# Performance work log

Hardware: AMD Instinct MI355X
Metric: run time of the kernel (lower is better)

Reference implementation:

```python
import jax, jax.numpy as jnp
import numpy as np

B, NPG, A, E = 128, 512, 8, 504   # graphs, nodes/graph, agents, edges/graph
F_IN, HID, H = 3, 64, 8
C = HID
F = H * C                          # 512 = concat head output
OUT = 2
NEG_SLOPE = 0.2


def _seg_softmax(alpha, dst, n):
    # edge-softmax normalized over destination-node neighborhoods
    m = jax.ops.segment_max(alpha, dst, num_segments=n)
    e = jnp.exp(alpha - m[dst])
    s = jax.ops.segment_sum(e, dst, num_segments=n)
    return e / jnp.clip(s[dst], 1e-16)


def _gat(x, src, dst, ea, W, b, a_s, a_d, We, a_e, n, self_loops):
    # PyG GATConv: heads=H, concat=True, edge_dim=1, fill_value='mean'
    xs = (x @ W).reshape(n, H, C)                      # [N,H,C]
    als = jnp.einsum('nhc,hc->nh', xs, a_s)            # alpha_src per node
    ald = jnp.einsum('nhc,hc->nh', xs, a_d)            # alpha_dst per node
    if self_loops:
        # fill_value='mean': self-loop attr = mean of incoming edge attrs
        ssum = jax.ops.segment_sum(ea, dst, num_segments=n)
        cnt = jax.ops.segment_sum(jnp.ones((dst.shape[0], 1), ea.dtype), dst, num_segments=n)
        loop_attr = ssum / jnp.maximum(cnt, 1.0)
        ea = jnp.concatenate([ea, loop_attr], axis=0)
        loop = jnp.arange(n, dtype=src.dtype)
        src = jnp.concatenate([src, loop])
        dst = jnp.concatenate([dst, loop])
    ee = (ea @ We).reshape(-1, H, C)                   # lin_edge
    ale = jnp.einsum('ehc,hc->eh', ee, a_e)            # alpha_edge per edge
    alpha = jax.nn.leaky_relu(als[src] + ald[dst] + ale, NEG_SLOPE)  # [E,H]
    alpha = _seg_softmax(alpha, dst, n)
    out = jax.ops.segment_sum(alpha[:, :, None] * xs[src], dst, num_segments=n)
    return out.reshape(n, H * C) + b


def _forward(x, edge_index, edge_attr, p1, p2, p3, fc1_w, fc1_b, fc2_w, fc2_b):
    Bq, npg, _ = x.shape
    n = Bq * npg
    off = (jnp.arange(Bq, dtype=edge_index.dtype) * npg)[:, None]   # PyG Batch offsets
    src = (edge_index[..., 0] + off).reshape(-1)
    dst = (edge_index[..., 1] + off).reshape(-1)
    ea = edge_attr.reshape(-1, 1)
    h = x.reshape(n, -1)
    h = jax.nn.relu(_gat(h, src, dst, ea, *p1, n, False))   # conv1: add_self_loops=False
    h = jax.nn.relu(_gat(h, src, dst, ea, *p2, n, True))
    h = jax.nn.relu(_gat(h, src, dst, ea, *p3, n, True))
    hg = h.reshape(Bq, npg, F)
    graph_emb = hg.mean(axis=1)                      # global_mean_pool (equal-size graphs)
    agent_emb = hg[:, :A].reshape(Bq * A, F)         # first num_agents nodes per graph
    comb = jnp.concatenate([agent_emb, jnp.repeat(graph_emb, A, axis=0)], axis=1)
    comb = jax.nn.relu(comb @ fc1_w + fc1_b)         # fc1 ReLU (extra torch.relu is idempotent)
    pred = comb @ fc2_w + fc2_b
    return pred.reshape(Bq, A, OUT)


def setup_inputs() -> dict:
    key = jax.random.key(0)
    ks = jax.random.split(key, 32)
    rn = lambda i, shape: jax.random.normal(ks[i], shape, jnp.float32) * 0.05
    inp = {
        'x': jax.random.normal(ks[0], (B, NPG, F_IN), jnp.float32),
        'edge_index': jax.random.randint(ks[1], (B, E, 2), 0, NPG, jnp.int32),
        'edge_attr': jax.random.normal(ks[2], (B, E, 1), jnp.float32),
    }
    dims = [F_IN, F, F]
    for li, din in enumerate(dims, start=1):
        inp[f'W{li}'] = rn(3 + li * 6, (din, H * C))
        inp[f'b{li}'] = jnp.zeros((H * C,), jnp.float32)
        inp[f'as{li}'] = rn(4 + li * 6, (H, C))
        inp[f'ad{li}'] = rn(5 + li * 6, (H, C))
        inp[f'We{li}'] = rn(6 + li * 6, (1, H * C))
        inp[f'ae{li}'] = rn(7 + li * 6, (H, C))
    inp['fc1_w'] = rn(28, (2 * F, 4 * HID))
    inp['fc1_b'] = jnp.zeros((4 * HID,), jnp.float32)
    inp['fc2_w'] = rn(29, (4 * HID, OUT))
    inp['fc2_b'] = jnp.zeros((OUT,), jnp.float32)
    return inp


def reference(x, edge_index, edge_attr,
              W1, b1, as1, ad1, We1, ae1,
              W2, b2, as2, ad2, We2, ae2,
              W3, b3, as3, ad3, We3, ae3,
              fc1_w, fc1_b, fc2_w, fc2_b):
    p1 = (W1, b1, as1, ad1, We1, ae1)
    p2 = (W2, b2, as2, ad2, We2, ae2)
    p3 = (W3, b3, as3, ad3, We3, ae3)
    return _forward(x, edge_index, edge_attr, p1, p2, p3, fc1_w, fc1_b, fc2_w, fc2_b)
```

## Files before the change

kernel.cpp:

```cpp
#include <hip/hip_runtime.h>
#include <hip/hip_bf16.h>
#include <math.h>

#define NGRAPH 128
#define NPG_   512
#define NN     (NGRAPH*NPG_)
#define EPG    504
#define ETOT   (NGRAPH*EPG)
#define HEADS  8
#define FDIM   512
#define NEG    0.2f

typedef __hip_bfloat16 bf16;
typedef __attribute__((ext_vector_type(8))) short short8;
typedef __attribute__((ext_vector_type(4))) float f32x4;

static __device__ __forceinline__ float bf(short s){
  union { unsigned u; float f; } c; c.u = ((unsigned)(unsigned short)s) << 16; return c.f;
}
static __device__ __forceinline__ short fbf(float v){
  bf16 b = __float2bfloat16(v); return *(short*)&b;
}

static __device__ __forceinline__ void gload16(void* lds, const void* g){
  __builtin_amdgcn_global_load_lds((const __attribute__((address_space(1))) void*)g,
                                   (__attribute__((address_space(3))) void*)lds, 16, 0, 0);
}

__global__ void k_sentinel(float* out, int n){
  int i = blockIdx.x*blockDim.x + threadIdx.x;
  if (i < n) out[i] = 12345.0f;
}

__global__ __launch_bounds__(512) void k_csr(const int* __restrict__ ei, const float* __restrict__ ea,
                                             const float* __restrict__ We0, const float* __restrict__ ae0,
                                             const float* __restrict__ We1, const float* __restrict__ ae1,
                                             const float* __restrict__ We2, const float* __restrict__ ae2,
                                             const float* __restrict__ W1,
                                             const float* __restrict__ as1, const float* __restrict__ ad1,
                                             const float* __restrict__ Wl2, const float* __restrict__ Wl3,
                                             int* __restrict__ deg_g, int* __restrict__ row_ptr,
                                             float* __restrict__ la,
                                             int* __restrict__ esrc, float* __restrict__ eattr,
                                             float* __restrict__ coef, float* __restrict__ wsd,
                                             bf16* __restrict__ wt){
  int b = blockIdx.x;
  int t = threadIdx.x;
  if (b >= NGRAPH){
    if (b < NGRAPH+3){
      int l = b - NGRAPH;
      const float* We = l==0 ? We0 : (l==1 ? We1 : We2);
      const float* ae = l==0 ? ae0 : (l==1 ? ae1 : ae2);
      float v = We[t]*ae[t];
      #pragma unroll
      for (int o=32;o>0;o>>=1) v += __shfl_down(v, o);
      if ((t & 63) == 0) coef[l*HEADS + (t>>6)] = v;
      return;
    }
    if (b == NGRAPH+3){
      float as_v = as1[t], ad_v = ad1[t];
      float v[6] = { W1[t]*as_v, W1[512+t]*as_v, W1[1024+t]*as_v,
                     W1[t]*ad_v, W1[512+t]*ad_v, W1[1024+t]*ad_v };
      #pragma unroll
      for (int o=32;o>0;o>>=1){
        #pragma unroll
        for (int q=0;q<6;q++) v[q] += __shfl_down(v[q], o);
      }
      if ((t & 63) == 0){
        int w = t >> 6;
        wsd[w*3+0]    = v[0]; wsd[w*3+1]    = v[1]; wsd[w*3+2]    = v[2];
        wsd[24+w*3+0] = v[3]; wsd[24+w*3+1] = v[4]; wsd[24+w*3+2] = v[5];
      }
      return;
    }
    int idx = (b - (NGRAPH+4))*512 + t;
    int l = idx >> 18;
    int r = idx & (FDIM*FDIM-1);
    int n = r >> 9, k = r & 511;
    const float* W = l ? Wl3 : Wl2;
    wt[idx] = __float2bfloat16(W[k*FDIM + n]);
    return;
  }
  __shared__ int   dg[512];
  __shared__ float ss[512];
  __shared__ int   scan[512];
  __shared__ int   cur[512];
  dg[t] = 0; ss[t] = 0.f;
  __syncthreads();
  int src=0, dst=0; float at=0.f;
  if (t < EPG){
    src = ei[(b*EPG+t)*2];
    dst = ei[(b*EPG+t)*2+1];
    at  = ea[b*EPG+t];
    atomicAdd(&dg[dst], 1);
    atomicAdd(&ss[dst], at);
  }
  __syncthreads();
  int d = dg[t];
  scan[t] = d;
  __syncthreads();
  for (int o=1;o<512;o<<=1){
    int v2 = (t>=o) ? scan[t-o] : 0;
    __syncthreads();
    scan[t] += v2;
    __syncthreads();
  }
  int excl = scan[t] - d;
  int n = b*NPG_ + t;
  row_ptr[n] = b*EPG + excl;
  deg_g[n]   = d;
  la[n]      = ss[t] / fmaxf((float)d, 1.f);
  cur[t] = excl;
  __syncthreads();
  if (t < EPG){
    int slot = atomicAdd(&cur[dst], 1);
    int p = b*EPG + slot;
    esrc[p]  = b*NPG_ + src;
    eattr[p] = at;
  }
}

__global__ __launch_bounds__(256) void k_gat1(const float* __restrict__ x,
                                              const float* __restrict__ W,
                                              const float* __restrict__ wsd,
                                              const float* __restrict__ coef,
                                              const int* __restrict__ row_ptr,
                                              const int* __restrict__ deg,
                                              const int* __restrict__ esrc,
                                              const float* __restrict__ eattr,
                                              const float* __restrict__ bias,
                                              bf16* __restrict__ h){
  int nwg = gridDim.x;
  int cpx = nwg >> 3;
  int bid = blockIdx.x;
  int swz = (bid & 7)*cpx + (bid >> 3);
  int n = swz*4 + (threadIdx.x >> 6);
  int lane = threadIdx.x & 63;
  int hh = lane >> 3;
  int f0 = lane << 3;

  float ws0 = wsd[hh*3+0],    ws1 = wsd[hh*3+1],    ws2 = wsd[hh*3+2];
  float wd0 = wsd[24+hh*3+0], wd1 = wsd[24+hh*3+1], wd2 = wsd[24+hh*3+2];
  float ch = coef[hh];

  const float* xr = x + n*3;
  float aldn = xr[0]*wd0 + xr[1]*wd1 + xr[2]*wd2;

  int row = row_ptr[n], d = deg[n];
  float m = -1e30f, ssum = 0.f;
  float a0 = 0.f, a1 = 0.f, a2 = 0.f;
  for (int i=0;i<d;i++){
    int s = esrc[row+i]; float at = eattr[row+i];
    const float* xsr = x + s*3;
    float y0 = xsr[0], y1 = xsr[1], y2 = xsr[2];
    float raw = y0*ws0 + y1*ws1 + y2*ws2 + aldn + at*ch;
    raw = raw > 0.f ? raw : NEG*raw;
    float mn = fmaxf(m, raw);
    float sc = __expf(m - mn);
    float p  = __expf(raw - mn);
    ssum = ssum*sc + p;
    a0 = a0*sc + p*y0;
    a1 = a1*sc + p*y1;
    a2 = a2*sc + p*y2;
    m = mn;
  }
  float inv = 1.f / fmaxf(ssum, 1e-16f);
  a0 *= inv; a1 *= inv; a2 *= inv;

  float w0[8], w1[8], w2[8], b8[8];
  #pragma unroll
  for (int j=0;j<8;j+=4){
    *(float4*)&w0[j] = *(const float4*)&W[f0+j];
    *(float4*)&w1[j] = *(const float4*)&W[FDIM+f0+j];
    *(float4*)&w2[j] = *(const float4*)&W[2*FDIM+f0+j];
    *(float4*)&b8[j] = *(const float4*)&bias[f0+j];
  }
  short8 r;
  #pragma unroll
  for (int j=0;j<8;j++){
    float o = a0*w0[j] + a1*w1[j] + a2*w2[j] + b8[j];
    r[j] = fbf(o > 0.f ? o : 0.f);
  }
  ((short8*)(h + (size_t)n*FDIM))[lane] = r;
}

__global__ __launch_bounds__(256) void k_gat(const bf16* __restrict__ xs,
                                             const float* __restrict__ als,
                                             const float* __restrict__ ald,
                                             const float* __restrict__ coef,
                                             const int* __restrict__ row_ptr,
                                             const int* __restrict__ deg,
                                             const int* __restrict__ esrc,
                                             const float* __restrict__ eattr,
                                             const float* __restrict__ la,
                                             const float* __restrict__ bias,
                                             bf16* __restrict__ h){
  int nwg = gridDim.x;
  int cpx = nwg >> 3;
  int bid = blockIdx.x;
  int swz = (bid & 7)*cpx + (bid >> 3);
  int n = swz*4 + (threadIdx.x >> 6);
  int lane = threadIdx.x & 63;
  int hh = lane >> 3;
  int row = row_ptr[n], d = deg[n];
  int tot = d + 1;
  float aldn = ald[n*HEADS+hh];
  float ch = coef[hh];
  float lan = la[n];

  float m = -1e30f, ssum = 0.f;
  float acc[8] = {};
  for (int i=0;i<tot;i++){
    int s; float at;
    if (i<d){ s = esrc[row+i]; at = eattr[row+i]; }
    else    { s = n;           at = lan; }
    float raw = als[s*HEADS+hh] + aldn + at*ch;
    raw = raw > 0.f ? raw : NEG*raw;
    float mn = fmaxf(m, raw);
    float scale = __expf(m - mn);
    float p = __expf(raw - mn);
    ssum = ssum*scale + p;
    short8 v = ((const short8*)(xs + (size_t)s*FDIM))[lane];
    #pragma unroll
    for (int j=0;j<8;j++) acc[j] = acc[j]*scale + p*bf(v[j]);
    m = mn;
  }
  float inv = 1.f / fmaxf(ssum, 1e-16f);
  const float4* b4 = (const float4*)bias;
  float4 ba = b4[lane*2], bb = b4[lane*2+1];
  float bias8[8] = {ba.x,ba.y,ba.z,ba.w,bb.x,bb.y,bb.z,bb.w};
  short8 r;
  #pragma unroll
  for (int j=0;j<8;j++){
    float o = acc[j]*inv + bias8[j];
    r[j] = fbf(o > 0.f ? o : 0.f);
  }
  ((short8*)(h + (size_t)n*FDIM))[lane] = r;
}

__global__ __launch_bounds__(256) void gemm_mfma(const bf16* __restrict__ A,
                                                 const bf16* __restrict__ Wt,
                                                 const float* __restrict__ a_s,
                                                 const float* __restrict__ a_d,
                                                 bf16* __restrict__ C,
                                                 float* __restrict__ als,
                                                 float* __restrict__ ald,
                                                 int M, int N, int K){
  __shared__ short smem[128*128];
  short* As = smem;
  short* Bs = smem + 128*64;
  int bid = blockIdx.x;
  int wk = ((bid & 7) << 8) | (bid >> 3);
  const int bm = (wk >> 2)*128, bn = (wk & 3)*128;
  const int tid = threadIdx.x;
  const int lane = tid & 63;
  const int w = tid >> 6;
  const int wm = (w >> 1)*64, wn = (w & 1)*64;
  const int lr = lane & 15;
  const int lk = lane >> 4;

  f32x4 acc[4][4] = {};

  for (int k0 = 0; k0 < K; k0 += 64){
    #pragma unroll
    for (int is = 0; is < 4; ++is){
      int i = is*256 + tid;
      int r = i >> 3, g = i & 7;
      int gs = g ^ (r & 7);
      gload16(&As[i*8], A  + (size_t)(bm+r)*K + k0 + gs*8);
      gload16(&Bs[i*8], Wt + (size_t)(bn+r)*K + k0 + gs*8);
    }
    __syncthreads();
    #pragma unroll
    for (int kk = 0; kk < 2; ++kk){
      short8 af[4], bfr[4];
      #pragma unroll
      for (int mi=0; mi<4; ++mi){
        int row = wm + mi*16 + lr;
        int g = (kk*4 + lk) ^ (row & 7);
        af[mi] = *(const short8*)&As[row*64 + g*8];
      }
      #pragma unroll
      for (int ni=0; ni<4; ++ni){
        int row = wn + ni*16 + lr;
        int g = (kk*4 + lk) ^ (row & 7);
        bfr[ni] = *(const short8*)&Bs[row*64 + g*8];
      }
      #pragma unroll
      for (int mi=0; mi<4; ++mi)
        #pragma unroll
        for (int ni=0; ni<4; ++ni)
          acc[mi][ni] = __builtin_amdgcn_mfma_f32_16x16x32_bf16(af[mi], bfr[ni], acc[mi][ni], 0,0,0);
    }
    __syncthreads();
  }

  int hh = (bn + wn) >> 6;
  float as_c[4], ad_c[4];
  #pragma unroll
  for (int ni=0; ni<4; ++ni){
    int c = hh*64 + ni*16 + lr;
    as_c[ni] = a_s[c];
    ad_c[ni] = a_d[c];
  }
  #pragma unroll
  for (int mi=0; mi<4; ++mi)
    #pragma unroll
    for (int r=0; r<4; ++r){
      float s = acc[mi][0][r]*as_c[0] + acc[mi][1][r]*as_c[1]
              + acc[mi][2][r]*as_c[2] + acc[mi][3][r]*as_c[3];
      float d = acc[mi][0][r]*ad_c[0] + acc[mi][1][r]*ad_c[1]
              + acc[mi][2][r]*ad_c[2] + acc[mi][3][r]*ad_c[3];
      #pragma unroll
      for (int o=1;o<16;o<<=1){ s += __shfl_xor(s, o); d += __shfl_xor(d, o); }
      if (lr == 0){
        int rowg = bm + wm + mi*16 + lk*4 + r;
        als[rowg*HEADS+hh] = s;
        ald[rowg*HEADS+hh] = d;
      }
    }

  short* Cs = smem;
  #pragma unroll
  for (int mi=0; mi<4; ++mi)
    #pragma unroll
    for (int ni=0; ni<4; ++ni){
      int col = wn + ni*16 + lr;
      int g = col >> 3, c3 = col & 7;
      #pragma unroll
      for (int r=0; r<4; ++r){
        int row = wm + mi*16 + lk*4 + r;
        Cs[row*128 + ((g ^ (row & 15))<<3) + c3] = fbf(acc[mi][ni][r]);
      }
    }
  __syncthreads();
  #pragma unroll
  for (int i2=0;i2<8;i2++){
    int id = (i2<<8) + tid;
    int row = id >> 4, seg = id & 15;
    int gg = seg ^ (row & 15);
    short8 v = *(const short8*)&Cs[row*128 + (gg<<3)];
    ((short8*)(C + (size_t)(bm+row)*N + bn))[seg] = v;
  }
}

__global__ __launch_bounds__(256) void k_gemb1(const bf16* __restrict__ h, float* __restrict__ pgemb){
  int gs_ = blockIdx.x;
  int g = gs_ >> 3, s = gs_ & 7;
  int t = threadIdx.x;
  int c = t & 63, rg = t >> 6;
  const bf16* base = h + ((size_t)(g*NPG_ + s*64 + rg*16))*FDIM;
  float acc[8] = {};
  #pragma unroll 4
  for (int i=0;i<16;i++){
    short8 v = ((const short8*)(base + (size_t)i*FDIM))[c];
    #pragma unroll
    for (int j=0;j<8;j++) acc[j] += bf(v[j]);
  }
  float* dst = pgemb + ((size_t)(gs_*4 + rg))*FDIM + c*8;
  float4 lo = {acc[0],acc[1],acc[2],acc[3]};
  float4 hi = {acc[4],acc[5],acc[6],acc[7]};
  *(float4*)dst = lo;
  *(float4*)(dst+4) = hi;
}

__global__ __launch_bounds__(256) void k_head1(const bf16* __restrict__ h,
                                               const float* __restrict__ pgemb,
                                               const float* __restrict__ fc1w,
                                               float* __restrict__ pf1,
                                               float* __restrict__ pge){
  __shared__ float ge[64];
  __shared__ float ag[8][64];
  int blk = blockIdx.x;
  int g = blk >> 3, q = blk & 7;
  int t = threadIdx.x;
  int k0 = q*64;

  if (t < 64){
    float s = 0.f;
    const float* p = pgemb + ((size_t)g*32)*FDIM + k0 + t;
    #pragma unroll 8
    for (int c=0;c<32;c++) s += p[(size_t)c*FDIM];
    ge[t] = s * (1.f/NPG_);
  } else if (t < 128){
    int i = t - 64;
    int r = i >> 3, c8 = i & 7;
    short8 v = ((const short8*)(h + ((size_t)(g*NPG_ + r))*FDIM + k0))[c8];
    #pragma unroll
    for (int j=0;j<8;j++) ag[r][c8*8+j] = bf(v[j]);
  }
  __syncthreads();

  float acc[8] = {};
  float gacc = 0.f;
  for (int kk=0; kk<64; kk++){
    float wa = fc1w[(size_t)(k0+kk)*256 + t];
    float wg = fc1w[(size_t)(FDIM+k0+kk)*256 + t];
    #pragma unroll
    for (int r=0;r<8;r++) acc[r] += ag[r][kk]*wa;
    gacc += ge[kk]*wg;
  }
  #pragma unroll
  for (int r=0;r<8;r++) pf1[((size_t)q*1024 + g*8 + r)*256 + t] = acc[r];
  pge[((size_t)q*NGRAPH + g)*256 + t] = gacc;
}

__global__ __launch_bounds__(256) void k_fc2(const float* __restrict__ pf1,
                                             const float* __restrict__ pge,
                                             const float* __restrict__ fc1b,
                                             const float* __restrict__ fc2w,
                                             const float* __restrict__ fc2b,
                                             float* __restrict__ out){
  __shared__ float f1[8][256];
  int g = blockIdx.x, t = threadIdx.x;
  float ges = 0.f;
  #pragma unroll
  for (int q=0;q<8;q++) ges += pge[((size_t)q*NGRAPH + g)*256 + t];
  float b = fc1b[t] + ges;
  #pragma unroll
  for (int r=0;r<8;r++){
    float s = 0.f;
    #pragma unroll
    for (int q=0;q<8;q++) s += pf1[((size_t)q*1024 + g*8 + r)*256 + t];
    f1[r][t] = fmaxf(s + b, 0.f);
  }
  __syncthreads();
  if (t < 128){
    int r = t >> 4, o = (t >> 3) & 1, l = t & 7;
    float s = 0.f;
    for (int k = l; k < 256; k += 8) s += f1[r][k] * fc2w[k*2+o];
    #pragma unroll
    for (int off=4; off; off>>=1) s += __shfl_down(s, off);
    if (l == 0) out[(g*8 + r)*2 + o] = s + fc2b[o];
  }
}

extern "C" void kernel_launch(void* const* d_in, const int* in_sizes, int n_in,
                              void* d_out, int out_size, void* d_ws, size_t ws_size,
                              hipStream_t stream)
{
  const float* x    = (const float*)d_in[0];
  const int*   ei   = (const int*)  d_in[1];
  const float* ea   = (const float*)d_in[2];
  const float* Wl[3]  = {(const float*)d_in[3],  (const float*)d_in[9],  (const float*)d_in[15]};
  const float* Bl[3]  = {(const float*)d_in[4],  (const float*)d_in[10], (const float*)d_in[16]};
  const float* ASl[3] = {(const float*)d_in[5],  (const float*)d_in[11], (const float*)d_in[17]};
  const float* ADl[3] = {(const float*)d_in[6],  (const float*)d_in[12], (const float*)d_in[18]};
  const float* WEl[3] = {(const float*)d_in[7],  (const float*)d_in[13], (const float*)d_in[19]};
  const float* AEl[3] = {(const float*)d_in[8],  (const float*)d_in[14], (const float*)d_in[20]};
  const float* FC1W = (const float*)d_in[21];
  const float* FC1B = (const float*)d_in[22];
  const float* FC2W = (const float*)d_in[23];
  const float* FC2B = (const float*)d_in[24];
  float* out = (float*)d_out;
  (void)in_sizes; (void)n_in;

  char* ws = (char*)d_ws;
  size_t off = 0;
  auto alloc = [&](size_t bytes)->char*{
    char* p = ws + off;
    off = (off + bytes + 255) & ~(size_t)255;
    return p;
  };
  bf16*  h       = (bf16*) alloc((size_t)NN*FDIM*2);
  bf16*  xs      = (bf16*) alloc((size_t)NN*FDIM*2);
  float* als     = (float*)alloc((size_t)NN*HEADS*4);
  float* ald     = (float*)alloc((size_t)NN*HEADS*4);
  float* la      = (float*)alloc((size_t)NN*4);
  int*   deg     = (int*)  alloc((size_t)NN*4);
  int*   row_ptr = (int*)  alloc((size_t)NN*4);
  int*   esrc    = (int*)  alloc((size_t)ETOT*4);
  float* eattr   = (float*)alloc((size_t)ETOT*4);
  float* coef    = (float*)alloc(3*HEADS*4);
  float* wsd     = (float*)alloc(48*4);
  bf16*  wt      = (bf16*) alloc((size_t)2*FDIM*FDIM*2);
  float* pgemb   = (float*)alloc((size_t)NGRAPH*32*FDIM*4);
  float* pf1     = (float*)alloc((size_t)8*1024*256*4);
  float* pge     = (float*)alloc((size_t)8*NGRAPH*256*4);

  if (off > ws_size){
    k_sentinel<<<(out_size+255)/256, 256, 0, stream>>>(out, out_size);
    return;
  }

  k_csr<<<NGRAPH+4+1024, 512, 0, stream>>>(ei, ea, WEl[0], AEl[0], WEl[1], AEl[1], WEl[2], AEl[2],
                                           Wl[0], ASl[0], ADl[0], Wl[1], Wl[2],
                                           deg, row_ptr, la, esrc, eattr, coef, wsd, wt);

  k_gat1<<<NN/4, 256, 0, stream>>>(x, Wl[0], wsd, coef, row_ptr, deg, esrc, eattr, Bl[0], h);

  for (int l=1;l<3;l++){
    gemm_mfma<<<2048, 256, 0, stream>>>(h, wt + (size_t)(l-1)*FDIM*FDIM,
                                        ASl[l], ADl[l], xs, als, ald, NN, FDIM, FDIM);
    k_gat<<<NN/4, 256, 0, stream>>>(xs, als, ald, coef + l*HEADS, row_ptr, deg, esrc, eattr, la, Bl[l], h);
  }

  k_gemb1<<<NGRAPH*8, 256, 0, stream>>>(h, pgemb);
  k_head1<<<NGRAPH*8, 256, 0, stream>>>(h, pgemb, FC1W, pf1, pge);
  k_fc2 <<<NGRAPH, 256, 0, stream>>>(pf1, pge, FC1B, FC2W, FC2B, out);
}
```

Baseline: 236.1 us.

## Double-buffer larger GEMM tiles and move attention dot-products to a separate kernel

The GEMM now uses 256x256 tiles with 512 threads and a double-buffered 128KB dynamic LDS pipeline, so global loads for the next k-tile overlap the MFMA work, and it raises MFMA priority while issuing. The fused alpha_src/alpha_dst epilogue and the LDS-staged coalesced store are removed. Stores now go straight from registers as scattered 2-byte writes, and a new per-node kernel rereads xs to compute the attention scalars. This trades an extra launch and an extra full pass over xs for a simpler, better-overlapped GEMM main loop.

```diff
diff --git a/kernel.cpp b/kernel.cpp
--- a/kernel.cpp
+++ b/kernel.cpp
@@ -184,6 +184,31 @@
   ((short8*)(h + (size_t)n*FDIM))[lane] = r;
 }
 
+__global__ __launch_bounds__(256) void k_attn_node(const bf16* __restrict__ xs,
+                                                   const float* __restrict__ a_s,
+                                                   const float* __restrict__ a_d,
+                                                   float* __restrict__ als,
+                                                   float* __restrict__ ald){
+  int n = blockIdx.x*4 + (threadIdx.x >> 6);
+  int lane = threadIdx.x & 63;
+  short8 v = ((const short8*)(xs + (size_t)n*FDIM))[lane];
+  const float4* as4 = (const float4*)a_s;
+  const float4* ad4 = (const float4*)a_d;
+  float4 sa = as4[lane*2], sb = as4[lane*2+1];
+  float4 da = ad4[lane*2], db = ad4[lane*2+1];
+  float s = bf(v[0])*sa.x + bf(v[1])*sa.y + bf(v[2])*sa.z + bf(v[3])*sa.w
+          + bf(v[4])*sb.x + bf(v[5])*sb.y + bf(v[6])*sb.z + bf(v[7])*sb.w;
+  float d = bf(v[0])*da.x + bf(v[1])*da.y + bf(v[2])*da.z + bf(v[3])*da.w
+          + bf(v[4])*db.x + bf(v[5])*db.y + bf(v[6])*db.z + bf(v[7])*db.w;
+  #pragma unroll
+  for (int o=1;o<8;o<<=1){ s += __shfl_xor(s, o); d += __shfl_xor(d, o); }
+  if ((lane & 7) == 0){
+    int hh = lane >> 3;
+    als[n*HEADS+hh] = s;
+    ald[n*HEADS+hh] = d;
+  }
+}
+
 __global__ __launch_bounds__(256) void k_gat(const bf16* __restrict__ xs,
                                              const float* __restrict__ als,
                                              const float* __restrict__ ald,
@@ -238,110 +263,88 @@
   ((short8*)(h + (size_t)n*FDIM))[lane] = r;
 }
 
-__global__ __launch_bounds__(256) void gemm_mfma(const bf16* __restrict__ A,
-                                                 const bf16* __restrict__ Wt,
-                                                 const float* __restrict__ a_s,
-                                                 const float* __restrict__ a_d,
-                                                 bf16* __restrict__ C,
-                                                 float* __restrict__ als,
-                                                 float* __restrict__ ald,
-                                                 int M, int N, int K){
-  __shared__ short smem[128*128];
-  short* As = smem;
-  short* Bs = smem + 128*64;
+__global__ __launch_bounds__(512, 2) void gemm_mfma(const bf16* __restrict__ A,
+                                                    const bf16* __restrict__ Wt,
+                                                    bf16* __restrict__ C,
+                                                    int M, int N, int K){
+  extern __shared__ short smem[];
   int bid = blockIdx.x;
-  int wk = ((bid & 7) << 8) | (bid >> 3);
-  const int bm = (wk >> 2)*128, bn = (wk & 3)*128;
+  int wk = ((bid & 7) << 6) | (bid >> 3);
+  const int bm = (wk >> 1)*256, bn = (wk & 1)*256;
   const int tid = threadIdx.x;
   const int lane = tid & 63;
   const int w = tid >> 6;
-  const int wm = (w >> 1)*64, wn = (w & 1)*64;
+  const int wm = (w >> 2)*128;
+  const int wn = (w & 3)*64;
   const int lr = lane & 15;
   const int lk = lane >> 4;
 
-  f32x4 acc[4][4] = {};
-
-  for (int k0 = 0; k0 < K; k0 += 64){
-    #pragma unroll
-    for (int is = 0; is < 4; ++is){
-      int i = is*256 + tid;
+  f32x4 acc[8][4] = {};
+  const int nt = K >> 6;
+
+  auto STAGE = [&](int s, int t){
+    short* Al = smem + s*32768;
+    short* Bl = smem + s*32768 + 16384;
+    int k0 = t << 6;
+    #pragma unroll
+    for (int ph=0; ph<4; ++ph){
+      int i = ph*512 + tid;
       int r = i >> 3, g = i & 7;
       int gs = g ^ (r & 7);
-      gload16(&As[i*8], A  + (size_t)(bm+r)*K + k0 + gs*8);
-      gload16(&Bs[i*8], Wt + (size_t)(bn+r)*K + k0 + gs*8);
+      gload16(&Al[i*8], A  + (size_t)(bm+r)*K + k0 + gs*8);
+      gload16(&Bl[i*8], Wt + (size_t)(bn+r)*K + k0 + gs*8);
     }
-    __syncthreads();
-    #pragma unroll
-    for (int kk = 0; kk < 2; ++kk){
-      short8 af[4], bfr[4];
+  };
+
+  STAGE(0, 0);
+  for (int t = 0; t < nt; ++t){
+    int s = t & 1;
+    if (t+1 < nt){
+      STAGE(s^1, t+1);
+      asm volatile("s_waitcnt vmcnt(8)" ::: "memory");
+    } else {
+      asm volatile("s_waitcnt vmcnt(0)" ::: "memory");
+    }
+    __builtin_amdgcn_s_barrier();
+    const short* Al = smem + s*32768;
+    const short* Bl = smem + s*32768 + 16384;
+    #pragma unroll
+    for (int kk=0; kk<2; ++kk){
+      short8 af[8], bfr[4];
       #pragma unroll
-      for (int mi=0; mi<4; ++mi){
+      for (int mi=0; mi<8; ++mi){
         int row = wm + mi*16 + lr;
-        int g = (kk*4 + lk) ^ (row & 7);
-        af[mi] = *(const short8*)&As[row*64 + g*8];
+        af[mi] = *(const short8*)&Al[row*64 + (((kk<<2)|lk) ^ (row&7))*8];
       }
       #pragma unroll
       for (int ni=0; ni<4; ++ni){
         int row = wn + ni*16 + lr;
-        int g = (kk*4 + lk) ^ (row & 7);
-        bfr[ni] = *(const short8*)&Bs[row*64 + g*8];
+        bfr[ni] = *(const short8*)&Bl[row*64 + (((kk<<2)|lk) ^ (row&7))*8];
       }
+      asm volatile("s_waitcnt lgkmcnt(0)" ::: "memory");
+      __builtin_amdgcn_sched_barrier(0);
+      __builtin_amdgcn_s_setprio(1);
       #pragma unroll
-      for (int mi=0; mi<4; ++mi)
+      for (int mi=0; mi<8; ++mi)
         #pragma unroll
         for (int ni=0; ni<4; ++ni)
           acc[mi][ni] = __builtin_amdgcn_mfma_f32_16x16x32_bf16(af[mi], bfr[ni], acc[mi][ni], 0,0,0);
+      __builtin_amdgcn_s_setprio(0);
     }
-    __syncthreads();
-  }
-
-  int hh = (bn + wn) >> 6;
-  float as_c[4], ad_c[4];
-  #pragma unroll
-  for (int ni=0; ni<4; ++ni){
-    int c = hh*64 + ni*16 + lr;
-    as_c[ni] = a_s[c];
-    ad_c[ni] = a_d[c];
-  }
-  #pragma unroll
-  for (int mi=0; mi<4; ++mi)
-    #pragma unroll
-    for (int r=0; r<4; ++r){
-      float s = acc[mi][0][r]*as_c[0] + acc[mi][1][r]*as_c[1]
-              + acc[mi][2][r]*as_c[2] + acc[mi][3][r]*as_c[3];
-      float d = acc[mi][0][r]*ad_c[0] + acc[mi][1][r]*ad_c[1]
-              + acc[mi][2][r]*ad_c[2] + acc[mi][3][r]*ad_c[3];
+    __builtin_amdgcn_s_barrier();
+  }
+
+  #pragma unroll
+  for (int mi=0; mi<8; ++mi)
+    #pragma unroll
+    for (int ni=0; ni<4; ++ni){
+      int col = bn + wn + ni*16 + lr;
       #pragma unroll
-      for (int o=1;o<16;o<<=1){ s += __shfl_xor(s, o); d += __shfl_xor(d, o); }
-      if (lr == 0){
+      for (int r=0; r<4; ++r){
         int rowg = bm + wm + mi*16 + lk*4 + r;
-        als[rowg*HEADS+hh] = s;
-        ald[rowg*HEADS+hh] = d;
+        C[(size_t)rowg*N + col] = __float2bfloat16(acc[mi][ni][r]);
       }
     }
-
-  short* Cs = smem;
-  #pragma unroll
-  for (int mi=0; mi<4; ++mi)
-    #pragma unroll
-    for (int ni=0; ni<4; ++ni){
-      int col = wn + ni*16 + lr;
-      int g = col >> 3, c3 = col & 7;
-      #pragma unroll
-      for (int r=0; r<4; ++r){
-        int row = wm + mi*16 + lk*4 + r;
-        Cs[row*128 + ((g ^ (row & 15))<<3) + c3] = fbf(acc[mi][ni][r]);
-      }
-    }
-  __syncthreads();
-  #pragma unroll
-  for (int i2=0;i2<8;i2++){
-    int id = (i2<<8) + tid;
-    int row = id >> 4, seg = id & 15;
-    int gg = seg ^ (row & 15);
-    short8 v = *(const short8*)&Cs[row*128 + (gg<<3)];
-    ((short8*)(C + (size_t)(bm+row)*N + bn))[seg] = v;
-  }
 }
 
 __global__ __launch_bounds__(256) void k_gemb1(const bf16* __restrict__ h, float* __restrict__ pgemb){
@@ -483,6 +486,9 @@
     return;
   }
 
+  (void)hipFuncSetAttribute((const void*)gemm_mfma,
+                            hipFuncAttributeMaxDynamicSharedMemorySize, 131072);
+
   k_csr<<<NGRAPH+4+1024, 512, 0, stream>>>(ei, ea, WEl[0], AEl[0], WEl[1], AEl[1], WEl[2], AEl[2],
                                            Wl[0], ASl[0], ADl[0], Wl[1], Wl[2],
                                            deg, row_ptr, la, esrc, eattr, coef, wsd, wt);
@@ -490,8 +496,8 @@
   k_gat1<<<NN/4, 256, 0, stream>>>(x, Wl[0], wsd, coef, row_ptr, deg, esrc, eattr, Bl[0], h);
 
   for (int l=1;l<3;l++){
-    gemm_mfma<<<2048, 256, 0, stream>>>(h, wt + (size_t)(l-1)*FDIM*FDIM,
-                                        ASl[l], ADl[l], xs, als, ald, NN, FDIM, FDIM);
+    gemm_mfma<<<512, 512, 131072, stream>>>(h, wt + (size_t)(l-1)*FDIM*FDIM, xs, NN, FDIM, FDIM);
+    k_attn_node<<<NN/4, 256, 0, stream>>>(xs, ASl[l], ADl[l], als, ald);
     k_gat<<<NN/4, 256, 0, stream>>>(xs, als, ald, coef + l*HEADS, row_ptr, deg, esrc, eattr, la, Bl[l], h);
   }
 
```

After: 235.0 us. Within noise of the previous version (-0.5%).
